# Optimization experiments

Measured on AMD Instinct MI355X. Metric: run time of the kernel, lower is better.

The kernel has to match this reference:

```python
import jax, jax.numpy as jnp
import numpy as np

NEG = -1e30  # log-space 'zero' (safe substitute for -inf)
EPS = 1e-7   # keras.backend.epsilon(), used by ctc_batch_cost


def _ctc_forward(logp, z, allow2):
    """CTC negative log-likelihood via the forward DP in log space.
    logp:   [B, T, C] log-probabilities
    z:      [B, S] extended label sequence (blanks interleaved), S = 2L+1
    allow2: [B, S] bool, whether the skip transition (s-2 -> s) is legal
    Returns [B, 1] loss (matches keras ctc_batch_cost output shape).
    """
    B, T, C = logp.shape
    S = z.shape[1]
    # Gather per-timestep log-probs of extended labels: [B, T, S] -> [T, B, S]
    b_idx = jnp.arange(B)[:, None, None]
    t_idx = jnp.arange(T)[None, :, None]
    lp_z = jnp.transpose(logp[b_idx, t_idx, z[:, None, :]], (1, 0, 2))

    s_idx = jnp.arange(S)[None, :]
    alpha0 = jnp.where(s_idx < 2, lp_z[0], NEG)  # paths may start at blank or first label

    def step(alpha, lp_t):
        a1 = jnp.concatenate([jnp.full((B, 1), NEG, alpha.dtype), alpha[:, :-1]], axis=1)
        a2 = jnp.concatenate([jnp.full((B, 2), NEG, alpha.dtype), alpha[:, :-2]], axis=1)
        a2 = jnp.where(allow2, a2, NEG)
        m = jnp.maximum(alpha, jnp.maximum(a1, a2))
        lse = m + jnp.log(jnp.exp(alpha - m) + jnp.exp(a1 - m) + jnp.exp(a2 - m))
        return lp_t + lse, None

    alphaT, _ = jax.lax.scan(step, alpha0, lp_z[1:])
    # Paths end at last blank (S-1) or last label (S-2)
    last, last2 = alphaT[:, -1], alphaT[:, -2]
    m = jnp.maximum(last, last2)
    ll = m + jnp.log(jnp.exp(last - m) + jnp.exp(last2 - m))
    return -ll[:, None]


def setup_inputs() -> dict:
    key = jax.random.key(0)
    k1, k2 = jax.random.split(key)
    B, T, C, L = 32, 2048, 256, 256
    # ctc_batch_cost expects post-softmax probabilities
    y_pred = jax.nn.softmax(jax.random.normal(k1, (B, T, C), jnp.float32), axis=-1)
    y_true = jax.random.randint(k2, (B, L), 0, C - 1)  # blank = C-1 excluded from labels
    return {"y_true": y_true, "y_pred": y_pred}


def reference(y_true, y_pred):
    B, T, C = y_pred.shape
    blank = C - 1
    L = y_true.shape[1]
    S = 2 * L + 1
    labels = y_true.astype(jnp.int32)
    # Extended label sequence: blank, l0, blank, l1, ..., blank
    z = jnp.full((B, S), blank, jnp.int32).at[:, 1::2].set(labels)
    z_m2 = jnp.concatenate([jnp.full((B, 2), -1, jnp.int32), z[:, :-2]], axis=1)
    allow2 = (z != blank) & (z != z_m2)
    logp = jnp.log(y_pred + EPS)
    return _ctc_forward(logp, z, allow2)
```

## Files before the change

kernel.cpp:

```cpp
#include <hip/hip_runtime.h>

#define TT   2048
#define CC   256
#define LL   256
#define SS   513
#define TM   1023
#define EPSF (1e-7f)
#define LN2F (0.69314718055994531f)
#define DPTH 8
#define RBTH 64
#define NCH  127
#define EMINI (-2000000000)
#define GSTR 260

#if __has_builtin(__builtin_amdgcn_frexp_expf)
#define FREXP_EXP __builtin_amdgcn_frexp_expf
#else
static __device__ __forceinline__ int FREXP_EXP(float x){ int e; return (frexpf(x,&e), e); }
#endif
#if __has_builtin(__builtin_amdgcn_ldexpf)
#define LDEXP __builtin_amdgcn_ldexpf
#else
#define LDEXP ldexpf
#endif

__launch_bounds__(256, 4)
__global__ void ctc_gather_kernel(const int* __restrict__ y_true,
                                  const float* __restrict__ y_pred,
                                  float* __restrict__ gat)
{
    const int b   = blockIdx.x;
    const int i   = threadIdx.x;
    const int col = y_true[b * LL + i];
    const float* rp = y_pred + (size_t)b * TT * CC;
    float*       gp = gat    + (size_t)b * TT * GSTR;
    const int tch = TT / gridDim.y;
    const int t0  = blockIdx.y * tch;
    #pragma unroll 4
    for (int t = t0; t < t0 + tch; ++t) {
        gp[(size_t)t * GSTR + i] = rp[(size_t)t * CC + col] + EPSF;
        if (i < 4)
            gp[(size_t)t * GSTR + 256 + i] = rp[(size_t)t * CC + (CC - 1)] + EPSF;
    }
}

__launch_bounds__(128, 1)
__global__ void ctc_fast_kernel(const int* __restrict__ y_true,
                                const float* __restrict__ y_pred,
                                const float* __restrict__ gat,
                                float* __restrict__ out)
{
    __shared__ float cw[SS];
    __shared__ int   ew[64];

    const int tid   = threadIdx.x;
    const int w     = tid >> 6;
    const int lane  = tid & 63;
    const int b     = blockIdx.x;
    const int blank = CC - 1;

    const int*   lab   = y_true + b * LL;
    const float* base  = y_pred + (size_t)b * TT * CC;
    const float* gLb   = gat    + (size_t)b * TT * GSTR;

    float kup[4];
    float kdn[4];
    const int col0 = lab[4 * lane];
    #pragma unroll
    for (int i = 0; i < 4; ++i) {
        const int li = 4 * lane + i;
        const int z  = lab[li];
        const int zm = (li >= 1) ? lab[li - 1] : -1;
        kup[i] = (z != zm) ? 1.0f : 0.0f;
        kdn[i] = (li <= 254 && lab[li + 1] != z) ? 1.0f : 0.0f;
    }

    float f[9];
    #pragma unroll
    for (int j = 0; j < 9; ++j) f[j] = 0.0f;
    int  e = 0;
    bool lzero;

    if (w == 0) {
        if (lane == 0) {
            f[0] = base[blank] + EPSF;
            f[1] = base[col0]  + EPSF;
        }
        lzero = (lane != 0);
    } else {
        if (lane == 63) {
            const float* rT = base + (size_t)(TT - 1) * CC;
            f[7] = rT[lab[255]] + EPSF;
            f[8] = rT[blank]    + EPSF;
        }
        lzero = (lane != 63);
    }

    auto renorm = [&]() {
        float m = fmaxf(fmaxf(fmaxf(f[0], f[1]), fmaxf(f[2], f[3])),
                        fmaxf(fmaxf(f[4], f[5]), fmaxf(f[6], fmaxf(f[7], f[8]))));
        const int em = FREXP_EXP(m);
        #pragma unroll
        for (int j = 0; j < 9; ++j) f[j] = LDEXP(f[j], -em);
        e += em;
    };

    auto fwd_step = [&](float pb, float p0, float p1, float p2, float p3) {
        float u7 = __shfl_up(f[7], 1);
        int   ue = __shfl_up(e, 1);
        if (lane == 0) { u7 = 0.0f; ue = e; }
        const int  dlt = ue - e;
        const bool rb  = lzero || (dlt >= RBTH);
        const int  sh  = rb ? -dlt : 0;
        #pragma unroll
        for (int j = 0; j < 9; ++j) f[j] = LDEXP(f[j], sh);
        e = rb ? ue : e;
        const int dlt2 = rb ? 0 : dlt;
        lzero = lzero && (u7 == 0.0f);
        const float bf = LDEXP(u7, dlt2);
        const float n0 = (f[0] + bf) * pb;
        const float n1 = (f[1] + f[0] + bf   * kup[0]) * p0;
        const float n2 = (f[2] + f[1]) * pb;
        const float n3 = (f[3] + f[2] + f[1] * kup[1]) * p1;
        const float n4 = (f[4] + f[3]) * pb;
        const float n5 = (f[5] + f[4] + f[3] * kup[2]) * p2;
        const float n6 = (f[6] + f[5]) * pb;
        const float n7 = (f[7] + f[6] + f[5] * kup[3]) * p3;
        const float n8 = (f[8] + f[7]) * pb;
        f[0]=n0; f[1]=n1; f[2]=n2; f[3]=n3; f[4]=n4;
        f[5]=n5; f[6]=n6; f[7]=n7; f[8]=n8;
    };

    auto bwd_step = [&](float pb, float p0, float p1, float p2, float p3) {
        float d1 = __shfl_down(f[1], 1);
        int   de = __shfl_down(e, 1);
        if (lane == 63) { d1 = 0.0f; de = e; }
        const int  dlt = de - e;
        const bool rb  = lzero || (dlt >= RBTH);
        const int  sh  = rb ? -dlt : 0;
        #pragma unroll
        for (int j = 0; j < 9; ++j) f[j] = LDEXP(f[j], sh);
        e = rb ? de : e;
        const int dlt2 = rb ? 0 : dlt;
        lzero = lzero && (d1 == 0.0f);
        const float bf = LDEXP(d1, dlt2);
        const float n0 = (f[0] + f[1]) * pb;
        const float n1 = (f[1] + f[2] + f[3] * kdn[0]) * p0;
        const float n2 = (f[2] + f[3]) * pb;
        const float n3 = (f[3] + f[4] + f[5] * kdn[1]) * p1;
        const float n4 = (f[4] + f[5]) * pb;
        const float n5 = (f[5] + f[6] + f[7] * kdn[2]) * p2;
        const float n6 = (f[6] + f[7]) * pb;
        const float n7 = (f[7] + f[8] + bf   * kdn[3]) * p3;
        const float n8 = (f[8] + bf) * pb;
        f[0]=n0; f[1]=n1; f[2]=n2; f[3]=n3; f[4]=n4;
        f[5]=n5; f[6]=n6; f[7]=n7; f[8]=n8;
    };

    float4 pf[DPTH];
    float  pbf[DPTH];
    const int bofs = 256 + (lane & 3);
    #pragma unroll
    for (int k = 0; k < DPTH; ++k) {
        const int r = (w == 0) ? (1 + k) : (TT - 2 - k);
        const float* rp = gLb + (size_t)r * GSTR;
        pf[k]  = *(const float4*)(rp + 4 * lane);
        pbf[k] = rp[bofs];
    }

    if (w == 0) {
        const float* gs = gLb + (size_t)(1 + DPTH) * GSTR;
        for (int c = 0; c < NCH; ++c) {
            #pragma unroll
            for (int k = 0; k < DPTH; ++k) {
                const float4 c4 = pf[k];
                const float  cb = pbf[k];
                pf[k]  = *(const float4*)(gs + 4 * lane);
                pbf[k] = gs[bofs];
                gs += GSTR;
                __builtin_amdgcn_sched_barrier(0);
                fwd_step(cb, c4.x, c4.y, c4.z, c4.w);
                if (k == 3 || k == 7) renorm();
            }
        }
        #pragma unroll
        for (int k = 0; k < 7; ++k) {
            fwd_step(pbf[k], pf[k].x, pf[k].y, pf[k].z, pf[k].w);
            if (k == 3) renorm();
        }
    } else {
        const float* gs = gLb + (size_t)(TT - 2 - DPTH) * GSTR;
        for (int c = 0; c < NCH; ++c) {
            #pragma unroll
            for (int k = 0; k < DPTH; ++k) {
                const float4 c4 = pf[k];
                const float  cb = pbf[k];
                pf[k]  = *(const float4*)(gs + 4 * lane);
                pbf[k] = gs[bofs];
                gs -= GSTR;
                __builtin_amdgcn_sched_barrier(0);
                bwd_step(cb, c4.x, c4.y, c4.z, c4.w);
                if (k == 3 || k == 7) renorm();
            }
        }
        #pragma unroll
        for (int k = 0; k < 7; ++k) {
            bwd_step(pbf[k], pf[k].x, pf[k].y, pf[k].z, pf[k].w);
            if (k == 3) renorm();
        }

        float d1 = __shfl_down(f[1], 1);
        int   de = __shfl_down(e, 1);
        if (lane == 63) { d1 = 0.0f; de = e; }
        int dlt = de - e;
        if (dlt >= RBTH) {
            #pragma unroll
            for (int j = 0; j < 9; ++j) f[j] = LDEXP(f[j], -dlt);
            e = de; dlt = 0;
        }
        const float bf = LDEXP(d1, dlt);
        float cb[9];
        cb[0] = f[0] + f[1];
        cb[1] = f[1] + f[2] + f[3] * kdn[0];
        cb[2] = f[2] + f[3];
        cb[3] = f[3] + f[4] + f[5] * kdn[1];
        cb[4] = f[4] + f[5];
        cb[5] = f[5] + f[6] + f[7] * kdn[2];
        cb[6] = f[6] + f[7];
        cb[7] = f[7] + f[8] + bf   * kdn[3];
        cb[8] = f[8] + bf;

        #pragma unroll
        for (int j = 0; j < 8; ++j) cw[8 * lane + j] = cb[j];
        if (lane == 63) cw[512] = cb[8];
        ew[lane] = e;
    }

    __syncthreads();

    if (w == 0) {
        float part = 0.0f;
        #pragma unroll
        for (int j = 0; j < 8; ++j) part += f[j] * cw[8 * lane + j];
        if (lane == 63) part += f[8] * cw[512];
        int   ep = (part > 0.0f) ? (e + ew[lane]) : EMINI;
        float m  = part;
        #pragma unroll
        for (int d = 1; d < 64; d <<= 1) {
            const float mo = __shfl_xor(m, d);
            const int   eo = __shfl_xor(ep, d);
            const int   E  = ep > eo ? ep : eo;
            m  = LDEXP(m, ep - E) + LDEXP(mo, eo - E);
            ep = E;
        }
        if (lane == 0)
            out[b] = -LN2F * ((float)ep + __builtin_amdgcn_logf(m));
    }
}

__launch_bounds__(128, 1)
__global__ void ctc_fb_kernel(const int* __restrict__ y_true,
                              const float* __restrict__ y_pred,
                              float* __restrict__ out)
{
    __shared__ float cw[SS];
    __shared__ int   ew[64];

    const int tid   = threadIdx.x;
    const int w     = tid >> 6;
    const int lane  = tid & 63;
    const int b     = blockIdx.x;
    const int blank = CC - 1;

    const int*   lab  = y_true + b * LL;
    const float* base = y_pred + (size_t)b * TT * CC;

    int   col[4];
    float kup[4], kdn[4];
    #pragma unroll
    for (int i = 0; i < 4; ++i) {
        const int li = 4 * lane + i;
        const int z  = lab[li];
        col[i] = z;
        const int zm = (li >= 1) ? lab[li - 1] : -1;
        kup[i] = (z != zm) ? 1.0f : 0.0f;
        kdn[i] = (li <= 254 && lab[li + 1] != z) ? 1.0f : 0.0f;
    }

    float f[9];
    #pragma unroll
    for (int j = 0; j < 9; ++j) f[j] = 0.0f;
    int  e = 0;
    bool lzero;

    if (w == 0) {
        if (lane == 0) { f[0] = base[blank] + EPSF; f[1] = base[col[0]] + EPSF; }
        lzero = (lane != 0);
    } else {
        if (lane == 63) {
            const float* rT = base + (size_t)(TT - 1) * CC;
            f[7] = rT[col[3]] + EPSF; f[8] = rT[blank] + EPSF;
        }
        lzero = (lane != 63);
    }

    float pfb[DPTH]; float pfl[DPTH][4];
    #pragma unroll
    for (int k = 0; k < DPTH; ++k) {
        const int r = (w == 0) ? (1 + k) : (TT - 2 - k);
        const float* rp = base + (size_t)r * CC;
        pfb[k] = rp[blank];
        #pragma unroll
        for (int i = 0; i < 4; ++i) pfl[k][i] = rp[col[i]];
    }

    auto renorm = [&]() {
        float m = fmaxf(fmaxf(fmaxf(f[0], f[1]), fmaxf(f[2], f[3])),
                        fmaxf(fmaxf(f[4], f[5]), fmaxf(f[6], fmaxf(f[7], f[8]))));
        const int em = FREXP_EXP(m);
        #pragma unroll
        for (int j = 0; j < 9; ++j) f[j] = LDEXP(f[j], -em);
        e += em;
    };
    auto fwd_step = [&](float pb, float p0, float p1, float p2, float p3) {
        float u7 = __shfl_up(f[7], 1);
        int   ue = __shfl_up(e, 1);
        if (lane == 0) { u7 = 0.0f; ue = e; }
        int dlt = ue - e;
        const bool rb = lzero || (dlt >= RBTH);
        if (__ballot(rb)) {
            const int sh = rb ? -dlt : 0;
            #pragma unroll
            for (int j = 0; j < 9; ++j) f[j] = LDEXP(f[j], sh);
            e = rb ? ue : e; dlt = rb ? 0 : dlt;
            lzero = lzero && (u7 == 0.0f);
        }
        const float bf = LDEXP(u7, dlt);
        const float n0 = (f[0] + bf) * pb;
        const float n1 = (f[1] + f[0] + bf   * kup[0]) * p0;
        const float n2 = (f[2] + f[1]) * pb;
        const float n3 = (f[3] + f[2] + f[1] * kup[1]) * p1;
        const float n4 = (f[4] + f[3]) * pb;
        const float n5 = (f[5] + f[4] + f[3] * kup[2]) * p2;
        const float n6 = (f[6] + f[5]) * pb;
        const float n7 = (f[7] + f[6] + f[5] * kup[3]) * p3;
        const float n8 = (f[8] + f[7]) * pb;
        f[0]=n0; f[1]=n1; f[2]=n2; f[3]=n3; f[4]=n4;
        f[5]=n5; f[6]=n6; f[7]=n7; f[8]=n8;
    };
    auto bwd_step = [&](float pb, float p0, float p1, float p2, float p3) {
        float d1 = __shfl_down(f[1], 1);
        int   de = __shfl_down(e, 1);
        if (lane == 63) { d1 = 0.0f; de = e; }
        int dlt = de - e;
        const bool rb = lzero || (dlt >= RBTH);
        if (__ballot(rb)) {
            const int sh = rb ? -dlt : 0;
            #pragma unroll
            for (int j = 0; j < 9; ++j) f[j] = LDEXP(f[j], sh);
            e = rb ? de : e; dlt = rb ? 0 : dlt;
            lzero = lzero && (d1 == 0.0f);
        }
        const float bf = LDEXP(d1, dlt);
        const float n0 = (f[0] + f[1]) * pb;
        const float n1 = (f[1] + f[2] + f[3] * kdn[0]) * p0;
        const float n2 = (f[2] + f[3]) * pb;
        const float n3 = (f[3] + f[4] + f[5] * kdn[1]) * p1;
        const float n4 = (f[4] + f[5]) * pb;
        const float n5 = (f[5] + f[6] + f[7] * kdn[2]) * p2;
        const float n6 = (f[6] + f[7]) * pb;
        const float n7 = (f[7] + f[8] + bf   * kdn[3]) * p3;
        const float n8 = (f[8] + bf) * pb;
        f[0]=n0; f[1]=n1; f[2]=n2; f[3]=n3; f[4]=n4;
        f[5]=n5; f[6]=n6; f[7]=n7; f[8]=n8;
    };

    if (w == 0) {
        for (int c = 0; c < NCH; ++c) {
            #pragma unroll
            for (int k = 0; k < DPTH; ++k) {
                const float pb = pfb[k] + EPSF;
                const float p0 = pfl[k][0] + EPSF, p1 = pfl[k][1] + EPSF;
                const float p2 = pfl[k][2] + EPSF, p3 = pfl[k][3] + EPSF;
                int tp = 1 + c * DPTH + k + DPTH; if (tp > TM) tp = TM;
                const float* rp = base + (size_t)tp * CC;
                pfb[k] = rp[blank];
                #pragma unroll
                for (int i = 0; i < 4; ++i) pfl[k][i] = rp[col[i]];
                fwd_step(pb, p0, p1, p2, p3);
                if (k == 3 || k == 7) renorm();
            }
        }
        #pragma unroll
        for (int k = 0; k < 7; ++k) {
            fwd_step(pfb[k] + EPSF, pfl[k][0] + EPSF, pfl[k][1] + EPSF,
                     pfl[k][2] + EPSF, pfl[k][3] + EPSF);
            if (k == 3) renorm();
        }
    } else {
        for (int c = 0; c < NCH; ++c) {
            #pragma unroll
            for (int k = 0; k < DPTH; ++k) {
                const float pb = pfb[k] + EPSF;
                const float p0 = pfl[k][0] + EPSF, p1 = pfl[k][1] + EPSF;
                const float p2 = pfl[k][2] + EPSF, p3 = pfl[k][3] + EPSF;
                int tp = (TT - 2) - (c * DPTH + k) - DPTH; if (tp < TM + 1) tp = TM + 1;
                const float* rp = base + (size_t)tp * CC;
                pfb[k] = rp[blank];
                #pragma unroll
                for (int i = 0; i < 4; ++i) pfl[k][i] = rp[col[i]];
                bwd_step(pb, p0, p1, p2, p3);
                if (k == 3 || k == 7) renorm();
            }
        }
        #pragma unroll
        for (int k = 0; k < 7; ++k) {
            bwd_step(pfb[k] + EPSF, pfl[k][0] + EPSF, pfl[k][1] + EPSF,
                     pfl[k][2] + EPSF, pfl[k][3] + EPSF);
            if (k == 3) renorm();
        }

        float d1 = __shfl_down(f[1], 1);
        int   de = __shfl_down(e, 1);
        if (lane == 63) { d1 = 0.0f; de = e; }
        int dlt = de - e;
        if (dlt >= RBTH) {
            #pragma unroll
            for (int j = 0; j < 9; ++j) f[j] = LDEXP(f[j], -dlt);
            e = de; dlt = 0;
        }
        const float bf = LDEXP(d1, dlt);
        float cb[9];
        cb[0] = f[0] + f[1];
        cb[1] = f[1] + f[2] + f[3] * kdn[0];
        cb[2] = f[2] + f[3];
        cb[3] = f[3] + f[4] + f[5] * kdn[1];
        cb[4] = f[4] + f[5];
        cb[5] = f[5] + f[6] + f[7] * kdn[2];
        cb[6] = f[6] + f[7];
        cb[7] = f[7] + f[8] + bf   * kdn[3];
        cb[8] = f[8] + bf;
        #pragma unroll
        for (int j = 0; j < 8; ++j) cw[8 * lane + j] = cb[j];
        if (lane == 63) cw[512] = cb[8];
        ew[lane] = e;
    }

    __syncthreads();

    if (w == 0) {
        float part = 0.0f;
        #pragma unroll
        for (int j = 0; j < 8; ++j) part += f[j] * cw[8 * lane + j];
        if (lane == 63) part += f[8] * cw[512];
        int   ep = (part > 0.0f) ? (e + ew[lane]) : EMINI;
        float m  = part;
        #pragma unroll
        for (int d = 1; d < 64; d <<= 1) {
            const float mo = __shfl_xor(m, d);
            const int   eo = __shfl_xor(ep, d);
            const int   E  = ep > eo ? ep : eo;
            m  = LDEXP(m, ep - E) + LDEXP(mo, eo - E);
            ep = E;
        }
        if (lane == 0)
            out[b] = -LN2F * ((float)ep + __builtin_amdgcn_logf(m));
    }
}

extern "C" void kernel_launch(void* const* d_in, const int* in_sizes, int n_in,
                              void* d_out, int out_size, void* d_ws, size_t ws_size,
                              hipStream_t stream)
{
    const int*   y_true = (const int*)d_in[0];
    const float* y_pred = (const float*)d_in[1];
    float*       out    = (float*)d_out;
    const int B = in_sizes[0] / LL;

    const size_t need = (size_t)B * TT * GSTR * sizeof(float);
    if (ws_size >= need) {
        float* gat = (float*)d_ws;
        ctc_gather_kernel<<<dim3(B, 32), 256, 0, stream>>>(y_true, y_pred, gat);
        ctc_fast_kernel<<<B, 128, 0, stream>>>(y_true, y_pred, gat, out);
    } else {
        ctc_fb_kernel<<<B, 128, 0, stream>>>(y_true, y_pred, out);
    }
}
```

Baseline: 211.1 us.

## Batch four CTC time steps per cross-lane exchange using halo recomputation

Each lane now fetches eight neighbour states at once through one round of shuffles. It then advances four time steps locally over a 17-element window, recomputing the overlapping halo, so cross-lane shuffles and exponent realignment happen once per four steps instead of every step. Renormalisation moves to the end of each group, and prefetch becomes double-buffered groups of four rows that also load the neighbour's label probabilities. The cost is redundant arithmetic on the halo and more registers, which could hurt the already register-heavy single-wave schedule.

```diff
diff --git a/kernel.cpp b/kernel.cpp
--- a/kernel.cpp
+++ b/kernel.cpp
@@ -44,11 +44,119 @@
     }
 }
 
+template<int NSTEP>
+__device__ __forceinline__ void fwd_group(float (&f)[9], int &e, bool &mm,
+        const float (&kk)[8], int lane,
+        float4 o0, float4 o1, float4 o2, float4 o3,
+        float4 q0, float4 q1, float4 q2, float4 q3,
+        float b0, float b1, float b2, float b3)
+{
+    float h[8];
+    #pragma unroll
+    for (int j = 0; j < 8; ++j) h[j] = __shfl_up(f[j], 1);
+    int he = __shfl_up(e, 1);
+    if (lane == 0) {
+        he = e;
+        #pragma unroll
+        for (int j = 0; j < 8; ++j) h[j] = 0.0f;
+    }
+    const int E  = mm ? (e > he ? e : he) : he;
+    const int dh = he - E, dn = e - E;
+    float g[17];
+    #pragma unroll
+    for (int j = 0; j < 8; ++j) g[j] = LDEXP(h[j], dh);
+    #pragma unroll
+    for (int j = 0; j < 9; ++j) g[8 + j] = LDEXP(f[j], dn);
+    e = E;
+
+#define FSW(Q, O, B, LO) do {                                                 \
+        const float pv[8] = {Q.x,Q.y,Q.z,Q.w,O.x,O.y,O.z,O.w};                \
+        _Pragma("unroll")                                                     \
+        for (int i = 16; i >= (LO); --i) {                                    \
+            if (i & 1) g[i] = (g[i] + g[i-1] + g[i-2]*kk[(i-1)>>1])           \
+                              * pv[(i-1)>>1];                                 \
+            else       g[i] = (g[i] + g[i-1]) * (B);                          \
+        }                                                                     \
+    } while (0)
+
+    if (NSTEP == 4) {
+        FSW(q0,o0,b0,2); FSW(q1,o1,b1,4); FSW(q2,o2,b2,6); FSW(q3,o3,b3,8);
+    } else {
+        FSW(q0,o0,b0,4); FSW(q1,o1,b1,6); FSW(q2,o2,b2,8);
+    }
+#undef FSW
+
+    #pragma unroll
+    for (int j = 0; j < 9; ++j) f[j] = g[8 + j];
+    float mx = f[0];
+    #pragma unroll
+    for (int j = 1; j < 9; ++j) mx = fmaxf(mx, f[j]);
+    const int em = FREXP_EXP(mx);
+    #pragma unroll
+    for (int j = 0; j < 9; ++j) f[j] = LDEXP(f[j], -em);
+    e += em;
+    mm = (mx > 0.0f);
+}
+
+template<int NSTEP>
+__device__ __forceinline__ void bwd_group(float (&f)[9], int &e, bool &mm,
+        const float (&kk)[8], int lane,
+        float4 o0, float4 o1, float4 o2, float4 o3,
+        float4 q0, float4 q1, float4 q2, float4 q3,
+        float b0, float b1, float b2, float b3)
+{
+    float h[8];
+    #pragma unroll
+    for (int j = 0; j < 8; ++j) h[j] = __shfl_down(f[j + 1], 1);
+    int he = __shfl_down(e, 1);
+    if (lane == 63) {
+        he = e;
+        #pragma unroll
+        for (int j = 0; j < 8; ++j) h[j] = 0.0f;
+    }
+    const int E  = mm ? (e > he ? e : he) : he;
+    const int dh = he - E, dn = e - E;
+    float g[17];
+    #pragma unroll
+    for (int j = 0; j < 9; ++j) g[j] = LDEXP(f[j], dn);
+    #pragma unroll
+    for (int j = 0; j < 8; ++j) g[9 + j] = LDEXP(h[j], dh);
+    e = E;
+
+#define BSW(O, Q, B, HI) do {                                                 \
+        const float pv[8] = {O.x,O.y,O.z,O.w,Q.x,Q.y,Q.z,Q.w};                \
+        _Pragma("unroll")                                                     \
+        for (int i = 0; i <= (HI); ++i) {                                     \
+            if (i & 1) g[i] = (g[i] + g[i+1] + g[i+2]*kk[(i-1)>>1])           \
+                              * pv[(i-1)>>1];                                 \
+            else       g[i] = (g[i] + g[i+1]) * (B);                          \
+        }                                                                     \
+    } while (0)
+
+    if (NSTEP == 4) {
+        BSW(o0,q0,b0,14); BSW(o1,q1,b1,12); BSW(o2,q2,b2,10); BSW(o3,q3,b3,8);
+    } else {
+        BSW(o0,q0,b0,12); BSW(o1,q1,b1,10); BSW(o2,q2,b2,8);
+    }
+#undef BSW
+
+    #pragma unroll
+    for (int j = 0; j < 9; ++j) f[j] = g[j];
+    float mx = f[0];
+    #pragma unroll
+    for (int j = 1; j < 9; ++j) mx = fmaxf(mx, f[j]);
+    const int em = FREXP_EXP(mx);
+    #pragma unroll
+    for (int j = 0; j < 9; ++j) f[j] = LDEXP(f[j], -em);
+    e += em;
+    mm = (mx > 0.0f);
+}
+
 __launch_bounds__(128, 1)
-__global__ void ctc_fast_kernel(const int* __restrict__ y_true,
-                                const float* __restrict__ y_pred,
-                                const float* __restrict__ gat,
-                                float* __restrict__ out)
+__global__ void ctc_grp_kernel(const int* __restrict__ y_true,
+                               const float* __restrict__ y_pred,
+                               const float* __restrict__ gat,
+                               float* __restrict__ out)
 {
     __shared__ float cw[SS];
     __shared__ int   ew[64];
@@ -59,156 +167,114 @@
     const int b     = blockIdx.x;
     const int blank = CC - 1;
 
-    const int*   lab   = y_true + b * LL;
-    const float* base  = y_pred + (size_t)b * TT * CC;
-    const float* gLb   = gat    + (size_t)b * TT * GSTR;
-
-    float kup[4];
-    float kdn[4];
-    const int col0 = lab[4 * lane];
-    #pragma unroll
-    for (int i = 0; i < 4; ++i) {
-        const int li = 4 * lane + i;
-        const int z  = lab[li];
-        const int zm = (li >= 1) ? lab[li - 1] : -1;
-        kup[i] = (z != zm) ? 1.0f : 0.0f;
-        kdn[i] = (li <= 254 && lab[li + 1] != z) ? 1.0f : 0.0f;
+    const int*   lab  = y_true + b * LL;
+    const float* base = y_pred + (size_t)b * TT * CC;
+    const float* gLb  = gat    + (size_t)b * TT * GSTR;
+
+    float kk[8];
+    if (w == 0) {
+        #pragma unroll
+        for (int j = 0; j < 8; ++j) {
+            const int li  = 4 * lane - 4 + j;
+            const int lic = li < 0 ? 0 : li;
+            const int z   = lab[lic];
+            const int zm  = (li >= 1) ? lab[li - 1] : -1;
+            kk[j] = (li >= 0 && z != zm) ? 1.0f : 0.0f;
+        }
+    } else {
+        #pragma unroll
+        for (int j = 0; j < 8; ++j) {
+            const int li  = 4 * lane + j;
+            const int lic = li > 255 ? 255 : li;
+            const int z   = lab[lic];
+            kk[j] = (li <= 254 && lab[li + 1] != z) ? 1.0f : 0.0f;
+        }
     }
 
     float f[9];
     #pragma unroll
     for (int j = 0; j < 9; ++j) f[j] = 0.0f;
     int  e = 0;
-    bool lzero;
+    bool mm;
 
     if (w == 0) {
         if (lane == 0) {
-            f[0] = base[blank] + EPSF;
-            f[1] = base[col0]  + EPSF;
-        }
-        lzero = (lane != 0);
+            f[0] = base[blank]        + EPSF;
+            f[1] = base[lab[0]]       + EPSF;
+        }
+        mm = (lane == 0);
     } else {
         if (lane == 63) {
             const float* rT = base + (size_t)(TT - 1) * CC;
             f[7] = rT[lab[255]] + EPSF;
             f[8] = rT[blank]    + EPSF;
         }
-        lzero = (lane != 63);
-    }
-
-    auto renorm = [&]() {
-        float m = fmaxf(fmaxf(fmaxf(f[0], f[1]), fmaxf(f[2], f[3])),
-                        fmaxf(fmaxf(f[4], f[5]), fmaxf(f[6], fmaxf(f[7], f[8]))));
-        const int em = FREXP_EXP(m);
-        #pragma unroll
-        for (int j = 0; j < 9; ++j) f[j] = LDEXP(f[j], -em);
-        e += em;
-    };
-
-    auto fwd_step = [&](float pb, float p0, float p1, float p2, float p3) {
-        float u7 = __shfl_up(f[7], 1);
-        int   ue = __shfl_up(e, 1);
-        if (lane == 0) { u7 = 0.0f; ue = e; }
-        const int  dlt = ue - e;
-        const bool rb  = lzero || (dlt >= RBTH);
-        const int  sh  = rb ? -dlt : 0;
-        #pragma unroll
-        for (int j = 0; j < 9; ++j) f[j] = LDEXP(f[j], sh);
-        e = rb ? ue : e;
-        const int dlt2 = rb ? 0 : dlt;
-        lzero = lzero && (u7 == 0.0f);
-        const float bf = LDEXP(u7, dlt2);
-        const float n0 = (f[0] + bf) * pb;
-        const float n1 = (f[1] + f[0] + bf   * kup[0]) * p0;
-        const float n2 = (f[2] + f[1]) * pb;
-        const float n3 = (f[3] + f[2] + f[1] * kup[1]) * p1;
-        const float n4 = (f[4] + f[3]) * pb;
-        const float n5 = (f[5] + f[4] + f[3] * kup[2]) * p2;
-        const float n6 = (f[6] + f[5]) * pb;
-        const float n7 = (f[7] + f[6] + f[5] * kup[3]) * p3;
-        const float n8 = (f[8] + f[7]) * pb;
-        f[0]=n0; f[1]=n1; f[2]=n2; f[3]=n3; f[4]=n4;
-        f[5]=n5; f[6]=n6; f[7]=n7; f[8]=n8;
-    };
-
-    auto bwd_step = [&](float pb, float p0, float p1, float p2, float p3) {
-        float d1 = __shfl_down(f[1], 1);
-        int   de = __shfl_down(e, 1);
-        if (lane == 63) { d1 = 0.0f; de = e; }
-        const int  dlt = de - e;
-        const bool rb  = lzero || (dlt >= RBTH);
-        const int  sh  = rb ? -dlt : 0;
-        #pragma unroll
-        for (int j = 0; j < 9; ++j) f[j] = LDEXP(f[j], sh);
-        e = rb ? de : e;
-        const int dlt2 = rb ? 0 : dlt;
-        lzero = lzero && (d1 == 0.0f);
-        const float bf = LDEXP(d1, dlt2);
-        const float n0 = (f[0] + f[1]) * pb;
-        const float n1 = (f[1] + f[2] + f[3] * kdn[0]) * p0;
-        const float n2 = (f[2] + f[3]) * pb;
-        const float n3 = (f[3] + f[4] + f[5] * kdn[1]) * p1;
-        const float n4 = (f[4] + f[5]) * pb;
-        const float n5 = (f[5] + f[6] + f[7] * kdn[2]) * p2;
-        const float n6 = (f[6] + f[7]) * pb;
-        const float n7 = (f[7] + f[8] + bf   * kdn[3]) * p3;
-        const float n8 = (f[8] + bf) * pb;
-        f[0]=n0; f[1]=n1; f[2]=n2; f[3]=n3; f[4]=n4;
-        f[5]=n5; f[6]=n6; f[7]=n7; f[8]=n8;
-    };
-
-    float4 pf[DPTH];
-    float  pbf[DPTH];
+        mm = (lane == 63);
+    }
+
+    const int oofs = 4 * lane;
+    const int qofs = (w == 0) ? (4 * lane - 4 < 0 ? 0 : 4 * lane - 4)
+                              : (4 * lane + 4);
     const int bofs = 256 + (lane & 3);
-    #pragma unroll
-    for (int k = 0; k < DPTH; ++k) {
-        const int r = (w == 0) ? (1 + k) : (TT - 2 - k);
-        const float* rp = gLb + (size_t)r * GSTR;
-        pf[k]  = *(const float4*)(rp + 4 * lane);
-        pbf[k] = rp[bofs];
-    }
-
-    if (w == 0) {
-        const float* gs = gLb + (size_t)(1 + DPTH) * GSTR;
-        for (int c = 0; c < NCH; ++c) {
-            #pragma unroll
-            for (int k = 0; k < DPTH; ++k) {
-                const float4 c4 = pf[k];
-                const float  cb = pbf[k];
-                pf[k]  = *(const float4*)(gs + 4 * lane);
-                pbf[k] = gs[bofs];
-                gs += GSTR;
-                __builtin_amdgcn_sched_barrier(0);
-                fwd_step(cb, c4.x, c4.y, c4.z, c4.w);
-                if (k == 3 || k == 7) renorm();
-            }
-        }
-        #pragma unroll
-        for (int k = 0; k < 7; ++k) {
-            fwd_step(pbf[k], pf[k].x, pf[k].y, pf[k].z, pf[k].w);
-            if (k == 3) renorm();
-        }
-    } else {
-        const float* gs = gLb + (size_t)(TT - 2 - DPTH) * GSTR;
-        for (int c = 0; c < NCH; ++c) {
-            #pragma unroll
-            for (int k = 0; k < DPTH; ++k) {
-                const float4 c4 = pf[k];
-                const float  cb = pbf[k];
-                pf[k]  = *(const float4*)(gs + 4 * lane);
-                pbf[k] = gs[bofs];
-                gs -= GSTR;
-                __builtin_amdgcn_sched_barrier(0);
-                bwd_step(cb, c4.x, c4.y, c4.z, c4.w);
-                if (k == 3 || k == 7) renorm();
-            }
-        }
-        #pragma unroll
-        for (int k = 0; k < 7; ++k) {
-            bwd_step(pbf[k], pf[k].x, pf[k].y, pf[k].z, pf[k].w);
-            if (k == 3) renorm();
-        }
-
+    const int dstp = (w == 0) ? GSTR : -GSTR;
+
+    float4 s0o[4], s0q[4]; float s0b[4];
+    float4 s1o[4], s1q[4]; float s1b[4];
+
+#define LOADG(SO, SQ, SB, ROWP) do {                                          \
+        const float* _rp = (ROWP);                                            \
+        _Pragma("unroll")                                                     \
+        for (int k = 0; k < 4; ++k) {                                         \
+            SO[k] = *(const float4*)(_rp + oofs);                             \
+            SQ[k] = *(const float4*)(_rp + qofs);                             \
+            SB[k] = _rp[bofs];                                                \
+            _rp += dstp;                                                      \
+        }                                                                     \
+    } while (0)
+
+    const float* grow = (w == 0) ? (gLb + (size_t)1 * GSTR)
+                                 : (gLb + (size_t)2046 * GSTR);
+    LOADG(s0o, s0q, s0b, grow); grow += 4 * dstp;
+    LOADG(s1o, s1q, s1b, grow); grow += 4 * dstp;
+
+#define PROC(SO, SQ, SB, NS) do {                                             \
+        const float4 a0 = SO[0], a1 = SO[1], a2 = SO[2], a3 = SO[3];          \
+        const float4 p0 = SQ[0], p1 = SQ[1], p2 = SQ[2], p3 = SQ[3];          \
+        const float  c0 = SB[0], c1 = SB[1], c2 = SB[2], c3 = SB[3];          \
+        if (NS == 4) { LOADG(SO, SQ, SB, grow); grow += 4 * dstp; }           \
+        __builtin_amdgcn_sched_barrier(0);                                    \
+        if (w == 0) fwd_group<NS>(f, e, mm, kk, lane,                         \
+                        a0,a1,a2,a3, p0,p1,p2,p3, c0,c1,c2,c3);               \
+        else        bwd_group<NS>(f, e, mm, kk, lane,                         \
+                        a0,a1,a2,a3, p0,p1,p2,p3, c0,c1,c2,c3);               \
+    } while (0)
+
+    for (int c = 0; c < 127; ++c) {
+        PROC(s0o, s0q, s0b, 4);
+        PROC(s1o, s1q, s1b, 4);
+    }
+    {
+        const float4 a0 = s0o[0], a1 = s0o[1], a2 = s0o[2], a3 = s0o[3];
+        const float4 p0 = s0q[0], p1 = s0q[1], p2 = s0q[2], p3 = s0q[3];
+        const float  c0 = s0b[0], c1 = s0b[1], c2 = s0b[2], c3 = s0b[3];
+        if (w == 0) fwd_group<4>(f, e, mm, kk, lane,
+                        a0,a1,a2,a3, p0,p1,p2,p3, c0,c1,c2,c3);
+        else        bwd_group<4>(f, e, mm, kk, lane,
+                        a0,a1,a2,a3, p0,p1,p2,p3, c0,c1,c2,c3);
+    }
+    {
+        const float4 a0 = s1o[0], a1 = s1o[1], a2 = s1o[2], a3 = s1o[3];
+        const float4 p0 = s1q[0], p1 = s1q[1], p2 = s1q[2], p3 = s1q[3];
+        const float  c0 = s1b[0], c1 = s1b[1], c2 = s1b[2], c3 = s1b[3];
+        if (w == 0) fwd_group<3>(f, e, mm, kk, lane,
+                        a0,a1,a2,a3, p0,p1,p2,p3, c0,c1,c2,c3);
+        else        bwd_group<3>(f, e, mm, kk, lane,
+                        a0,a1,a2,a3, p0,p1,p2,p3, c0,c1,c2,c3);
+    }
+#undef PROC
+#undef LOADG
+
+    if (w == 1) {
         float d1 = __shfl_down(f[1], 1);
         int   de = __shfl_down(e, 1);
         if (lane == 63) { d1 = 0.0f; de = e; }
@@ -221,15 +287,14 @@
         const float bf = LDEXP(d1, dlt);
         float cb[9];
         cb[0] = f[0] + f[1];
-        cb[1] = f[1] + f[2] + f[3] * kdn[0];
+        cb[1] = f[1] + f[2] + f[3] * kk[0];
         cb[2] = f[2] + f[3];
-        cb[3] = f[3] + f[4] + f[5] * kdn[1];
+        cb[3] = f[3] + f[4] + f[5] * kk[1];
         cb[4] = f[4] + f[5];
-        cb[5] = f[5] + f[6] + f[7] * kdn[2];
+        cb[5] = f[5] + f[6] + f[7] * kk[2];
         cb[6] = f[6] + f[7];
-        cb[7] = f[7] + f[8] + bf   * kdn[3];
+        cb[7] = f[7] + f[8] + bf   * kk[3];
         cb[8] = f[8] + bf;
-
         #pragma unroll
         for (int j = 0; j < 8; ++j) cw[8 * lane + j] = cb[j];
         if (lane == 63) cw[512] = cb[8];
@@ -481,7 +546,7 @@
     if (ws_size >= need) {
         float* gat = (float*)d_ws;
         ctc_gather_kernel<<<dim3(B, 32), 256, 0, stream>>>(y_true, y_pred, gat);
-        ctc_fast_kernel<<<B, 128, 0, stream>>>(y_true, y_pred, gat, out);
+        ctc_grp_kernel<<<B, 128, 0, stream>>>(y_true, y_pred, gat, out);
     } else {
         ctc_fb_kernel<<<B, 128, 0, stream>>>(y_true, y_pred, out);
     }
```

Result: faster. 175.4 us, median of 2 (-17.0%).
